# Kernel optimization log

Hardware: AMD Instinct MI355X
Metric: run time of the kernel (lower is better)

## Reference

```python
import jax, jax.numpy as jnp
import numpy as np

B = 65536      # batch of scenarios
IN = 16        # input_size
HL = 10        # hl_dim
NL = 3         # hl_num
T = 200        # number of time points
NPOP = 8.6e6   # population N


def setup_inputs() -> dict:
    key = jax.random.key(0)
    k0, k1, k2, k3 = jax.random.split(key, 4)
    data = jax.random.normal(k0, (B, IN), dtype=jnp.float32)
    times = jnp.arange(T, dtype=jnp.float32)
    # stacked params for the 3 param nets (gamma, beta, I0); xavier-ish scale, zero bias
    W0 = jax.random.normal(k1, (3, HL, IN), dtype=jnp.float32) * np.float32(1.0 / np.sqrt(IN))
    b0 = jnp.zeros((3, HL), jnp.float32)
    Wh = jax.random.normal(k2, (3, NL, HL, HL), dtype=jnp.float32) * np.float32(1.0 / np.sqrt(HL))
    bh = jnp.zeros((3, NL, HL), jnp.float32)
    Wo = jax.random.normal(k3, (3, 1, HL), dtype=jnp.float32) * np.float32(1.0 / np.sqrt(HL))
    bo = jnp.zeros((3, 1), jnp.float32)
    return {"data": data, "times": times, "W0": W0, "b0": b0,
            "Wh": Wh, "bh": bh, "Wo": Wo, "bo": bo}


def _param_nets(x, W0, b0, Wh, bh, Wo, bo):
    # runs the 3 tiny MLPs in parallel over leading net axis n in {gamma, beta, I0}
    h = jnp.tanh(jnp.einsum('bi,nhi->nbh', x, W0) + b0[:, None, :])
    for l in range(Wh.shape[1]):
        h = jnp.tanh(jnp.einsum('nbh,nkh->nbk', h, Wh[:, l]) + bh[:, l][:, None, :])
    out = jnp.einsum('nbh,noh->nbo', h, Wo) + bo[:, None, :]   # [3, B, 1]
    return jax.nn.softplus(out[..., 0])                        # [3, B]


def _forward_sir(data, times, W0, b0, Wh, bh, Wo, bo):
    vals = _param_nets(data, W0, b0, Wh, bh, Wo, bo)
    gamma, beta, I0 = vals[0], vals[1], vals[2]   # each [B]
    S0 = NPOP - I0
    R0 = jnp.zeros_like(S0)
    x0 = jnp.stack([S0, I0, R0], axis=1)          # [B, 3]

    def rhs(x):
        S, I = x[:, 0], x[:, 1]
        flux = beta * S * I / NPOP
        rec = gamma * I
        return jnp.stack([-flux, flux - rec, rec], axis=1)

    def step(x, dt):
        # classic RK4 over each interval between consecutive time points
        k1 = rhs(x)
        k2 = rhs(x + 0.5 * dt * k1)
        k3 = rhs(x + 0.5 * dt * k2)
        k4 = rhs(x + dt * k3)
        xn = x + (dt / 6.0) * (k1 + 2.0 * k2 + 2.0 * k3 + k4)
        return xn, xn

    dts = times[1:] - times[:-1]                  # [T-1]
    _, ys = jax.lax.scan(step, x0, dts)           # [T-1, B, 3]
    ys = jnp.concatenate([x0[None], ys], axis=0)  # [T, B, 3]
    return ys[:, :, 1:2].reshape(-1, 1)           # infected compartment, (T*B, output_size=1)


def reference(data, times, W0, b0, Wh, bh, Wo, bo):
    return _forward_sir(data, times, W0, b0, Wh, bh, Wo, bo)
```

## Files before the change

### kernel.cpp

```cpp
#include <hip/hip_runtime.h>
#include <math.h>

#define BSZ   65536
#define INP   16
#define HL    10
#define NL    3
#define TT    200
#define NPOP  8600000.0f

#define NCH8  24

__device__ __forceinline__ float fast_tanh(float x) {
    float e = exp2f(x * 2.8853900817779268f);
    return 1.0f - 2.0f * __builtin_amdgcn_rcpf(e + 1.0f);
}

__global__ __launch_bounds__(256) void mlp_kernel(
    const float* __restrict__ data,
    const float* __restrict__ W0,
    const float* __restrict__ b0,
    const float* __restrict__ Wh,
    const float* __restrict__ bh,
    const float* __restrict__ Wo,
    const float* __restrict__ bo,
    float* __restrict__ vals)
{
    const int n   = blockIdx.y;
    const int tid = threadIdx.x;

    __shared__ float sW0[HL * INP];
    __shared__ float sb0[HL];
    __shared__ float sWh[NL * HL * HL];
    __shared__ float sbh[NL * HL];
    __shared__ float sWo[HL];
    __shared__ float sbo;

    for (int i = tid; i < HL * INP;      i += 256) sW0[i] = W0[n * HL * INP + i];
    for (int i = tid; i < HL;            i += 256) sb0[i] = b0[n * HL + i];
    for (int i = tid; i < NL * HL * HL;  i += 256) sWh[i] = Wh[n * NL * HL * HL + i];
    for (int i = tid; i < NL * HL;       i += 256) sbh[i] = bh[n * NL * HL + i];
    for (int i = tid; i < HL;            i += 256) sWo[i] = Wo[n * HL + i];
    if (tid == 0) sbo = bo[n];
    __syncthreads();

    const int b = blockIdx.x * 256 + tid;

    float x[INP];
    const float4* xin = reinterpret_cast<const float4*>(data + (size_t)b * INP);
    #pragma unroll
    for (int q = 0; q < INP / 4; ++q) {
        float4 v = xin[q];
        x[q * 4 + 0] = v.x; x[q * 4 + 1] = v.y;
        x[q * 4 + 2] = v.z; x[q * 4 + 3] = v.w;
    }

    float h[HL];
    #pragma unroll
    for (int k = 0; k < HL; ++k) {
        float acc = sb0[k];
        #pragma unroll
        for (int i = 0; i < INP; ++i)
            acc = fmaf(x[i], sW0[k * INP + i], acc);
        h[k] = fast_tanh(acc);
    }
    #pragma unroll
    for (int l = 0; l < NL; ++l) {
        float h2[HL];
        #pragma unroll
        for (int k = 0; k < HL; ++k) {
            float acc = sbh[l * HL + k];
            #pragma unroll
            for (int i = 0; i < HL; ++i)
                acc = fmaf(h[i], sWh[(l * HL + k) * HL + i], acc);
            h2[k] = fast_tanh(acc);
        }
        #pragma unroll
        for (int k = 0; k < HL; ++k) h[k] = h2[k];
    }
    float acc = sbo;
    #pragma unroll
    for (int i = 0; i < HL; ++i)
        acc = fmaf(h[i], sWo[i], acc);

    vals[(size_t)n * BSZ + b] = fmaxf(acc, 0.0f) + log1pf(expf(-fabsf(acc)));
}

__global__ __launch_bounds__(256, 1) void sir_kernel(
    const float* __restrict__ vals,
    const float* __restrict__ times,
    float* __restrict__ out)
{
    const int tid = threadIdx.x;
    const int b = blockIdx.x * 256 + tid;

    const float gamma = vals[b];
    const float beta  = vals[BSZ + b];
    const float I0    = vals[2 * BSZ + b];

    __shared__ float sdt[208];
    if (tid < TT - 1)       sdt[tid] = times[tid + 1] - times[tid];
    else if (tid < 208)     sdt[tid] = 0.0f;
    __syncthreads();

    float S = NPOP - I0;
    float I = I0;
    const float bn = beta * (1.0f / NPOP);

    out[b] = I;

    auto step = [&](float dt) {
        const float hdt = 0.5f * dt;
        float f1 = (bn * S) * I;
        float r1 = gamma * I;
        float m1 = f1 - r1;
        float aS = fmaf(-hdt, f1, S), aI = fmaf(hdt, m1, I);
        float f2 = (bn * aS) * aI;
        float r2 = gamma * aI;
        float m2 = f2 - r2;
        float bS = fmaf(-hdt, f2, S), bI = fmaf(hdt, m2, I);
        float f3 = (bn * bS) * bI;
        float r3 = gamma * bI;
        float m3 = f3 - r3;
        float cS = fmaf(-dt, f3, S),  cI = fmaf(dt, m3, I);
        float f4 = (bn * cS) * cI;
        float r4 = gamma * cI;
        float m4 = f4 - r4;
        const float c6 = dt * (1.0f / 6.0f);
        S = fmaf(-c6, (f1 + f4) + 2.0f * (f2 + f3), S);
        I = fmaf( c6, (m1 + m4) + 2.0f * (m2 + m3), I);
    };

    const float4* sdt4 = reinterpret_cast<const float4*>(sdt);

    float4 da = sdt4[0];
    float4 db = sdt4[1];
    float* op = out + BSZ;

    #pragma unroll 1
    for (int g = 0; g < NCH8; ++g) {
        float4 na = sdt4[2 * g + 2];
        float4 nb = sdt4[2 * g + 3];
        __builtin_amdgcn_sched_barrier(0);

        float ic0, ic1, ic2, ic3, ic4, ic5, ic6, ic7;
        step(da.x); ic0 = I; op[b          ] = ic0;
        step(da.y); ic1 = I; op[b + 1 * BSZ] = ic1;
        step(da.z); ic2 = I; op[b + 2 * BSZ] = ic2;
        step(da.w); ic3 = I; op[b + 3 * BSZ] = ic3;
        step(db.x); ic4 = I; op[b + 4 * BSZ] = ic4;
        step(db.y); ic5 = I; op[b + 5 * BSZ] = ic5;
        step(db.z); ic6 = I; op[b + 6 * BSZ] = ic6;
        step(db.w); ic7 = I; op[b + 7 * BSZ] = ic7;

        asm volatile("" :: "v"(ic0), "v"(ic1), "v"(ic2), "v"(ic3),
                           "v"(ic4), "v"(ic5), "v"(ic6), "v"(ic7));

        da = na; db = nb;
        op += 8 * BSZ;
    }

    {
        float d0 = sdt[192], d1 = sdt[193], d2 = sdt[194], d3 = sdt[195];
        float d4 = sdt[196], d5 = sdt[197], d6 = sdt[198];
        float ic0, ic1, ic2, ic3, ic4, ic5, ic6;
        step(d0); ic0 = I; op[b          ] = ic0;
        step(d1); ic1 = I; op[b + 1 * BSZ] = ic1;
        step(d2); ic2 = I; op[b + 2 * BSZ] = ic2;
        step(d3); ic3 = I; op[b + 3 * BSZ] = ic3;
        step(d4); ic4 = I; op[b + 4 * BSZ] = ic4;
        step(d5); ic5 = I; op[b + 5 * BSZ] = ic5;
        step(d6); ic6 = I; op[b + 6 * BSZ] = ic6;
        asm volatile("" :: "v"(ic0), "v"(ic1), "v"(ic2), "v"(ic3),
                           "v"(ic4), "v"(ic5), "v"(ic6));
    }
}

extern "C" void kernel_launch(void* const* d_in, const int* in_sizes, int n_in,
                              void* d_out, int out_size, void* d_ws, size_t ws_size,
                              hipStream_t stream) {
    const float* data  = (const float*)d_in[0];
    const float* times = (const float*)d_in[1];
    const float* W0    = (const float*)d_in[2];
    const float* b0    = (const float*)d_in[3];
    const float* Wh    = (const float*)d_in[4];
    const float* bh    = (const float*)d_in[5];
    const float* Wo    = (const float*)d_in[6];
    const float* bo    = (const float*)d_in[7];
    float* out  = (float*)d_out;
    float* vals = (float*)d_ws;

    dim3 gridA(BSZ / 256, 3);
    mlp_kernel<<<gridA, 256, 0, stream>>>(data, W0, b0, Wh, bh, Wo, bo, vals);
    sir_kernel<<<BSZ / 256, 256, 0, stream>>>(vals, times, out);
}
```

Baseline: 32.00 us.

## Double-buffer SIR output stores with inline-asm global stores and manual vmcnt waits

Replaces the 8-step store loop with two alternating 16-step banks. Each bank has precomputed per-row offsets and issues stores as inline-asm global_store_dword with an SGPR base. Explicit s_waitcnt vmcnt(16) lets up to 16 stores stay in flight while the next bank's RK4 steps compute, and per-store address arithmetic is removed. The cost is more VGPR pressure (32 offsets plus 32 held values) and fragile hand-managed memory counters and offset wraparound.

```diff
diff --git a/kernel.cpp b/kernel.cpp
--- a/kernel.cpp
+++ b/kernel.cpp
@@ -7,8 +7,7 @@
 #define NL    3
 #define TT    200
 #define NPOP  8600000.0f
-
-#define NCH8  24
+#define ROWB  (BSZ * 4u)
 
 __device__ __forceinline__ float fast_tanh(float x) {
     float e = exp2f(x * 2.8853900817779268f);
@@ -17,12 +16,9 @@
 
 __global__ __launch_bounds__(256) void mlp_kernel(
     const float* __restrict__ data,
-    const float* __restrict__ W0,
-    const float* __restrict__ b0,
-    const float* __restrict__ Wh,
-    const float* __restrict__ bh,
-    const float* __restrict__ Wo,
-    const float* __restrict__ bo,
+    const float* __restrict__ W0,  const float* __restrict__ b0,
+    const float* __restrict__ Wh,  const float* __restrict__ bh,
+    const float* __restrict__ Wo,  const float* __restrict__ bo,
     float* __restrict__ vals)
 {
     const int n   = blockIdx.y;
@@ -84,6 +80,16 @@
 
     vals[(size_t)n * BSZ + b] = fmaxf(acc, 0.0f) + log1pf(expf(-fabsf(acc)));
 }
+
+#define ST(VOFF, VAL) \
+    asm volatile("global_store_dword %0, %1, %2" \
+                 :: "v"(VOFF), "v"(VAL), "s"(out) : "memory")
+
+#define KEEP16(A) \
+    asm volatile("" :: "v"(A[0]),  "v"(A[1]),  "v"(A[2]),  "v"(A[3]),  \
+                       "v"(A[4]),  "v"(A[5]),  "v"(A[6]),  "v"(A[7]),  \
+                       "v"(A[8]),  "v"(A[9]),  "v"(A[10]), "v"(A[11]), \
+                       "v"(A[12]), "v"(A[13]), "v"(A[14]), "v"(A[15]))
 
 __global__ __launch_bounds__(256, 1) void sir_kernel(
     const float* __restrict__ vals,
@@ -132,47 +138,89 @@
 
     const float4* sdt4 = reinterpret_cast<const float4*>(sdt);
 
-    float4 da = sdt4[0];
-    float4 db = sdt4[1];
-    float* op = out + BSZ;
+    const unsigned vb = (unsigned)b * 4u;
+    unsigned voffA[16], voffB[16];
+    #pragma unroll
+    for (int k = 0; k < 16; ++k) {
+        voffA[k] = (unsigned)(k + 1  - 32) * ROWB + vb;
+        voffB[k] = (unsigned)(k + 17 - 32) * ROWB + vb;
+    }
+    float icA[16], icB[16];
+    #pragma unroll
+    for (int k = 0; k < 16; ++k) { icA[k] = 0.0f; icB[k] = 0.0f; }
+
+    float4 d0 = sdt4[0], d1 = sdt4[1], d2 = sdt4[2], d3 = sdt4[3];
+    float4 e0, e1, e2, e3;
 
     #pragma unroll 1
-    for (int g = 0; g < NCH8; ++g) {
-        float4 na = sdt4[2 * g + 2];
-        float4 nb = sdt4[2 * g + 3];
-        __builtin_amdgcn_sched_barrier(0);
-
-        float ic0, ic1, ic2, ic3, ic4, ic5, ic6, ic7;
-        step(da.x); ic0 = I; op[b          ] = ic0;
-        step(da.y); ic1 = I; op[b + 1 * BSZ] = ic1;
-        step(da.z); ic2 = I; op[b + 2 * BSZ] = ic2;
-        step(da.w); ic3 = I; op[b + 3 * BSZ] = ic3;
-        step(db.x); ic4 = I; op[b + 4 * BSZ] = ic4;
-        step(db.y); ic5 = I; op[b + 5 * BSZ] = ic5;
-        step(db.z); ic6 = I; op[b + 6 * BSZ] = ic6;
-        step(db.w); ic7 = I; op[b + 7 * BSZ] = ic7;
-
-        asm volatile("" :: "v"(ic0), "v"(ic1), "v"(ic2), "v"(ic3),
-                           "v"(ic4), "v"(ic5), "v"(ic6), "v"(ic7));
-
-        da = na; db = nb;
-        op += 8 * BSZ;
-    }
-
-    {
-        float d0 = sdt[192], d1 = sdt[193], d2 = sdt[194], d3 = sdt[195];
-        float d4 = sdt[196], d5 = sdt[197], d6 = sdt[198];
-        float ic0, ic1, ic2, ic3, ic4, ic5, ic6;
-        step(d0); ic0 = I; op[b          ] = ic0;
-        step(d1); ic1 = I; op[b + 1 * BSZ] = ic1;
-        step(d2); ic2 = I; op[b + 2 * BSZ] = ic2;
-        step(d3); ic3 = I; op[b + 3 * BSZ] = ic3;
-        step(d4); ic4 = I; op[b + 4 * BSZ] = ic4;
-        step(d5); ic5 = I; op[b + 5 * BSZ] = ic5;
-        step(d6); ic6 = I; op[b + 6 * BSZ] = ic6;
-        asm volatile("" :: "v"(ic0), "v"(ic1), "v"(ic2), "v"(ic3),
-                           "v"(ic4), "v"(ic5), "v"(ic6));
-    }
+    for (int j = 0; j < 6; ++j) {
+        asm volatile("s_waitcnt vmcnt(16)" ::: "memory");
+        KEEP16(icA);
+        __builtin_amdgcn_sched_barrier(0);
+        #pragma unroll
+        for (int k = 0; k < 16; ++k) voffA[k] += 32u * ROWB;
+        e0 = sdt4[8 * j + 4]; e1 = sdt4[8 * j + 5];
+        e2 = sdt4[8 * j + 6]; e3 = sdt4[8 * j + 7];
+        __builtin_amdgcn_sched_barrier(0);
+
+        step(d0.x); icA[0]  = I; ST(voffA[0],  icA[0]);
+        step(d0.y); icA[1]  = I; ST(voffA[1],  icA[1]);
+        step(d0.z); icA[2]  = I; ST(voffA[2],  icA[2]);
+        step(d0.w); icA[3]  = I; ST(voffA[3],  icA[3]);
+        step(d1.x); icA[4]  = I; ST(voffA[4],  icA[4]);
+        step(d1.y); icA[5]  = I; ST(voffA[5],  icA[5]);
+        step(d1.z); icA[6]  = I; ST(voffA[6],  icA[6]);
+        step(d1.w); icA[7]  = I; ST(voffA[7],  icA[7]);
+        step(d2.x); icA[8]  = I; ST(voffA[8],  icA[8]);
+        step(d2.y); icA[9]  = I; ST(voffA[9],  icA[9]);
+        step(d2.z); icA[10] = I; ST(voffA[10], icA[10]);
+        step(d2.w); icA[11] = I; ST(voffA[11], icA[11]);
+        step(d3.x); icA[12] = I; ST(voffA[12], icA[12]);
+        step(d3.y); icA[13] = I; ST(voffA[13], icA[13]);
+        step(d3.z); icA[14] = I; ST(voffA[14], icA[14]);
+        step(d3.w); icA[15] = I; ST(voffA[15], icA[15]);
+
+        asm volatile("s_waitcnt vmcnt(16)" ::: "memory");
+        KEEP16(icB);
+        __builtin_amdgcn_sched_barrier(0);
+        #pragma unroll
+        for (int k = 0; k < 16; ++k) voffB[k] += 32u * ROWB;
+        d0 = sdt4[8 * j + 8];  d1 = sdt4[8 * j + 9];
+        d2 = sdt4[8 * j + 10]; d3 = sdt4[8 * j + 11];
+        __builtin_amdgcn_sched_barrier(0);
+
+        step(e0.x); icB[0]  = I; ST(voffB[0],  icB[0]);
+        step(e0.y); icB[1]  = I; ST(voffB[1],  icB[1]);
+        step(e0.z); icB[2]  = I; ST(voffB[2],  icB[2]);
+        step(e0.w); icB[3]  = I; ST(voffB[3],  icB[3]);
+        step(e1.x); icB[4]  = I; ST(voffB[4],  icB[4]);
+        step(e1.y); icB[5]  = I; ST(voffB[5],  icB[5]);
+        step(e1.z); icB[6]  = I; ST(voffB[6],  icB[6]);
+        step(e1.w); icB[7]  = I; ST(voffB[7],  icB[7]);
+        step(e2.x); icB[8]  = I; ST(voffB[8],  icB[8]);
+        step(e2.y); icB[9]  = I; ST(voffB[9],  icB[9]);
+        step(e2.z); icB[10] = I; ST(voffB[10], icB[10]);
+        step(e2.w); icB[11] = I; ST(voffB[11], icB[11]);
+        step(e3.x); icB[12] = I; ST(voffB[12], icB[12]);
+        step(e3.y); icB[13] = I; ST(voffB[13], icB[13]);
+        step(e3.z); icB[14] = I; ST(voffB[14], icB[14]);
+        step(e3.w); icB[15] = I; ST(voffB[15], icB[15]);
+    }
+
+    asm volatile("s_waitcnt vmcnt(0)" ::: "memory");
+    KEEP16(icA);
+    KEEP16(icB);
+    __builtin_amdgcn_sched_barrier(0);
+    #pragma unroll
+    for (int k = 0; k < 7; ++k) voffA[k] += 32u * ROWB;
+
+    step(d0.x); icA[0] = I; ST(voffA[0], icA[0]);
+    step(d0.y); icA[1] = I; ST(voffA[1], icA[1]);
+    step(d0.z); icA[2] = I; ST(voffA[2], icA[2]);
+    step(d0.w); icA[3] = I; ST(voffA[3], icA[3]);
+    step(d1.x); icA[4] = I; ST(voffA[4], icA[4]);
+    step(d1.y); icA[5] = I; ST(voffA[5], icA[5]);
+    step(d1.z); icA[6] = I; ST(voffA[6], icA[6]);
 }
 
 extern "C" void kernel_launch(void* const* d_in, const int* in_sizes, int n_in,
```

Result: no change. 31.93 us (-0.2%).

## Stage SIR outputs through double-buffered LDS and emit dwordx4 global stores

Applied to the files above, without the earlier changes.

The SIR kernel now writes each thread's per-step infected value into a double-buffered shared-memory tile of 16 time steps. After a block barrier, each wave reads its transposed slice and issues 128-bit global stores through inline assembly, replacing per-step scalar 4-byte stores. The goal is fewer store instructions and wider memory transactions on this write-heavy kernel. In exchange it adds barriers, LDS traffic and hand-placed waitcnt fences whose correctness depends on exact counter accounting.

```diff
diff --git a/kernel.cpp b/kernel.cpp
--- a/kernel.cpp
+++ b/kernel.cpp
@@ -7,8 +7,11 @@
 #define NL    3
 #define TT    200
 #define NPOP  8600000.0f
-
-#define NCH8  24
+#define ROWB  (BSZ * 4u)
+#define CH    16
+#define NCH   12
+
+typedef float f32x4 __attribute__((ext_vector_type(4)));
 
 __device__ __forceinline__ float fast_tanh(float x) {
     float e = exp2f(x * 2.8853900817779268f);
@@ -17,12 +20,9 @@
 
 __global__ __launch_bounds__(256) void mlp_kernel(
     const float* __restrict__ data,
-    const float* __restrict__ W0,
-    const float* __restrict__ b0,
-    const float* __restrict__ Wh,
-    const float* __restrict__ bh,
-    const float* __restrict__ Wo,
-    const float* __restrict__ bo,
+    const float* __restrict__ W0,  const float* __restrict__ b0,
+    const float* __restrict__ Wh,  const float* __restrict__ bh,
+    const float* __restrict__ Wo,  const float* __restrict__ bo,
     float* __restrict__ vals)
 {
     const int n   = blockIdx.y;
@@ -85,28 +85,40 @@
     vals[(size_t)n * BSZ + b] = fmaxf(acc, 0.0f) + log1pf(expf(-fabsf(acc)));
 }
 
+#define ST4(VOFF, VAL) \
+    asm volatile("global_store_dwordx4 %0, %1, %2" \
+                 :: "v"(VOFF), "v"(VAL), "s"(out) : "memory")
+
 __global__ __launch_bounds__(256, 1) void sir_kernel(
     const float* __restrict__ vals,
     const float* __restrict__ times,
     float* __restrict__ out)
 {
     const int tid = threadIdx.x;
-    const int b = blockIdx.x * 256 + tid;
+    const int b   = blockIdx.x * 256 + tid;
+    const int w   = tid >> 6;
+    const int l   = tid & 63;
 
     const float gamma = vals[b];
     const float beta  = vals[BSZ + b];
     const float I0    = vals[2 * BSZ + b];
 
     __shared__ float sdt[208];
-    if (tid < TT - 1)       sdt[tid] = times[tid + 1] - times[tid];
-    else if (tid < 208)     sdt[tid] = 0.0f;
+    __shared__ float sbuf[2][CH][256];
+
+    if (tid < TT - 1)   sdt[tid] = times[tid + 1] - times[tid];
+    else if (tid < 208) sdt[tid] = 0.0f;
     __syncthreads();
 
     float S = NPOP - I0;
     float I = I0;
     const float bn = beta * (1.0f / NPOP);
 
-    out[b] = I;
+    {
+        unsigned v0 = (unsigned)b * 4u;
+        asm volatile("global_store_dword %0, %1, %2"
+                     :: "v"(v0), "v"(I), "s"(out) : "memory");
+    }
 
     auto step = [&](float dt) {
         const float hdt = 0.5f * dt;
@@ -132,47 +144,113 @@
 
     const float4* sdt4 = reinterpret_cast<const float4*>(sdt);
 
-    float4 da = sdt4[0];
-    float4 db = sdt4[1];
-    float* op = out + BSZ;
+    const unsigned colb = ((unsigned)blockIdx.x * 256u + 4u * (unsigned)l) * 4u;
+    unsigned voff0 = (unsigned)(4 * w + 1) * ROWB + colb;
+    unsigned voff1 = voff0 + ROWB;
+    unsigned voff2 = voff0 + 2u * ROWB;
+    unsigned voff3 = voff0 + 3u * ROWB;
+
+    float4 d0 = sdt4[0], d1 = sdt4[1], d2 = sdt4[2], d3 = sdt4[3];
+    float4 e0, e1, e2, e3;
 
     #pragma unroll 1
-    for (int g = 0; g < NCH8; ++g) {
-        float4 na = sdt4[2 * g + 2];
-        float4 nb = sdt4[2 * g + 3];
-        __builtin_amdgcn_sched_barrier(0);
-
-        float ic0, ic1, ic2, ic3, ic4, ic5, ic6, ic7;
-        step(da.x); ic0 = I; op[b          ] = ic0;
-        step(da.y); ic1 = I; op[b + 1 * BSZ] = ic1;
-        step(da.z); ic2 = I; op[b + 2 * BSZ] = ic2;
-        step(da.w); ic3 = I; op[b + 3 * BSZ] = ic3;
-        step(db.x); ic4 = I; op[b + 4 * BSZ] = ic4;
-        step(db.y); ic5 = I; op[b + 5 * BSZ] = ic5;
-        step(db.z); ic6 = I; op[b + 6 * BSZ] = ic6;
-        step(db.w); ic7 = I; op[b + 7 * BSZ] = ic7;
-
-        asm volatile("" :: "v"(ic0), "v"(ic1), "v"(ic2), "v"(ic3),
-                           "v"(ic4), "v"(ic5), "v"(ic6), "v"(ic7));
-
-        da = na; db = nb;
-        op += 8 * BSZ;
-    }
-
-    {
-        float d0 = sdt[192], d1 = sdt[193], d2 = sdt[194], d3 = sdt[195];
-        float d4 = sdt[196], d5 = sdt[197], d6 = sdt[198];
-        float ic0, ic1, ic2, ic3, ic4, ic5, ic6;
-        step(d0); ic0 = I; op[b          ] = ic0;
-        step(d1); ic1 = I; op[b + 1 * BSZ] = ic1;
-        step(d2); ic2 = I; op[b + 2 * BSZ] = ic2;
-        step(d3); ic3 = I; op[b + 3 * BSZ] = ic3;
-        step(d4); ic4 = I; op[b + 4 * BSZ] = ic4;
-        step(d5); ic5 = I; op[b + 5 * BSZ] = ic5;
-        step(d6); ic6 = I; op[b + 6 * BSZ] = ic6;
-        asm volatile("" :: "v"(ic0), "v"(ic1), "v"(ic2), "v"(ic3),
-                           "v"(ic4), "v"(ic5), "v"(ic6));
-    }
+    for (int cc = 0; cc < NCH / 2; ++cc) {
+        step(d0.x); sbuf[0][ 0][tid] = I;
+        step(d0.y); sbuf[0][ 1][tid] = I;
+        step(d0.z); sbuf[0][ 2][tid] = I;
+        step(d0.w); sbuf[0][ 3][tid] = I;
+        step(d1.x); sbuf[0][ 4][tid] = I;
+        step(d1.y); sbuf[0][ 5][tid] = I;
+        step(d1.z); sbuf[0][ 6][tid] = I;
+        step(d1.w); sbuf[0][ 7][tid] = I;
+        step(d2.x); sbuf[0][ 8][tid] = I;
+        step(d2.y); sbuf[0][ 9][tid] = I;
+        step(d2.z); sbuf[0][10][tid] = I;
+        step(d2.w); sbuf[0][11][tid] = I;
+        step(d3.x); sbuf[0][12][tid] = I;
+        step(d3.y); sbuf[0][13][tid] = I;
+        step(d3.z); sbuf[0][14][tid] = I;
+        step(d3.w); sbuf[0][15][tid] = I;
+
+        asm volatile("s_waitcnt lgkmcnt(0)" ::: "memory");
+        __builtin_amdgcn_sched_barrier(0);
+        __builtin_amdgcn_s_barrier();
+
+        e0 = sdt4[8 * cc + 4]; e1 = sdt4[8 * cc + 5];
+        e2 = sdt4[8 * cc + 6]; e3 = sdt4[8 * cc + 7];
+
+        asm volatile("s_waitcnt vmcnt(4)" ::: "memory");
+        __builtin_amdgcn_sched_barrier(0);
+
+        f32x4 sA0 = *(const f32x4*)&sbuf[0][4 * w + 0][4 * l];
+        f32x4 sA1 = *(const f32x4*)&sbuf[0][4 * w + 1][4 * l];
+        f32x4 sA2 = *(const f32x4*)&sbuf[0][4 * w + 2][4 * l];
+        f32x4 sA3 = *(const f32x4*)&sbuf[0][4 * w + 3][4 * l];
+        ST4(voff0, sA0);
+        ST4(voff1, sA1);
+        ST4(voff2, sA2);
+        ST4(voff3, sA3);
+        voff0 += CH * ROWB; voff1 += CH * ROWB;
+        voff2 += CH * ROWB; voff3 += CH * ROWB;
+
+        step(e0.x); sbuf[1][ 0][tid] = I;
+        step(e0.y); sbuf[1][ 1][tid] = I;
+        step(e0.z); sbuf[1][ 2][tid] = I;
+        step(e0.w); sbuf[1][ 3][tid] = I;
+        step(e1.x); sbuf[1][ 4][tid] = I;
+        step(e1.y); sbuf[1][ 5][tid] = I;
+        step(e1.z); sbuf[1][ 6][tid] = I;
+        step(e1.w); sbuf[1][ 7][tid] = I;
+        step(e2.x); sbuf[1][ 8][tid] = I;
+        step(e2.y); sbuf[1][ 9][tid] = I;
+        step(e2.z); sbuf[1][10][tid] = I;
+        step(e2.w); sbuf[1][11][tid] = I;
+        step(e3.x); sbuf[1][12][tid] = I;
+        step(e3.y); sbuf[1][13][tid] = I;
+        step(e3.z); sbuf[1][14][tid] = I;
+        step(e3.w); sbuf[1][15][tid] = I;
+
+        asm volatile("s_waitcnt lgkmcnt(0)" ::: "memory");
+        __builtin_amdgcn_sched_barrier(0);
+        __builtin_amdgcn_s_barrier();
+
+        d0 = sdt4[8 * cc + 8];  d1 = sdt4[8 * cc + 9];
+        d2 = sdt4[8 * cc + 10]; d3 = sdt4[8 * cc + 11];
+
+        asm volatile("s_waitcnt vmcnt(4)" ::: "memory");
+        __builtin_amdgcn_sched_barrier(0);
+
+        f32x4 sB0 = *(const f32x4*)&sbuf[1][4 * w + 0][4 * l];
+        f32x4 sB1 = *(const f32x4*)&sbuf[1][4 * w + 1][4 * l];
+        f32x4 sB2 = *(const f32x4*)&sbuf[1][4 * w + 2][4 * l];
+        f32x4 sB3 = *(const f32x4*)&sbuf[1][4 * w + 3][4 * l];
+        ST4(voff0, sB0);
+        ST4(voff1, sB1);
+        ST4(voff2, sB2);
+        ST4(voff3, sB3);
+        voff0 += CH * ROWB; voff1 += CH * ROWB;
+        voff2 += CH * ROWB; voff3 += CH * ROWB;
+    }
+
+    step(d0.x); sbuf[0][0][tid] = I;
+    step(d0.y); sbuf[0][1][tid] = I;
+    step(d0.z); sbuf[0][2][tid] = I;
+    step(d0.w); sbuf[0][3][tid] = I;
+    step(d1.x); sbuf[0][4][tid] = I;
+    step(d1.y); sbuf[0][5][tid] = I;
+    step(d1.z); sbuf[0][6][tid] = I;
+
+    asm volatile("s_waitcnt lgkmcnt(0)" ::: "memory");
+    __builtin_amdgcn_sched_barrier(0);
+    __builtin_amdgcn_s_barrier();
+
+    asm volatile("s_waitcnt vmcnt(4)" ::: "memory");
+    __builtin_amdgcn_sched_barrier(0);
+
+    if (4 * w + 0 < 7) { f32x4 v = *(const f32x4*)&sbuf[0][4 * w + 0][4 * l]; ST4(voff0, v); }
+    if (4 * w + 1 < 7) { f32x4 v = *(const f32x4*)&sbuf[0][4 * w + 1][4 * l]; ST4(voff1, v); }
+    if (4 * w + 2 < 7) { f32x4 v = *(const f32x4*)&sbuf[0][4 * w + 2][4 * l]; ST4(voff2, v); }
+    if (4 * w + 3 < 7) { f32x4 v = *(const f32x4*)&sbuf[0][4 * w + 3][4 * l]; ST4(voff3, v); }
 }
 
 extern "C" void kernel_launch(void* const* d_in, const int* in_sizes, int n_in,
```

Result: slower. 32.91 us (+2.8%).

## Fold beta/N into SIR state, shrink SIR blocks to one wave, fast softplus

Applied to the files above, without the earlier changes.

The RK4 step now tracks P = beta/N * S instead of S, so each flux is a single multiply and the recovery term folds into an FMA. This cuts the per-stage instruction count. SIR blocks drop from 256 to 64 threads (one wavefront) to spread 1024 blocks across CUs, and softplus uses exp2/log2 intrinsics. The initial store uses inline asm with a 32-bit offset, and the reformulation slightly changes floating-point rounding.

```diff
diff --git a/kernel.cpp b/kernel.cpp
--- a/kernel.cpp
+++ b/kernel.cpp
@@ -15,14 +15,16 @@
     return 1.0f - 2.0f * __builtin_amdgcn_rcpf(e + 1.0f);
 }
 
+__device__ __forceinline__ float fast_softplus(float x) {
+    float t = exp2f(-fabsf(x) * 1.4426950408889634f);
+    return fmaxf(x, 0.0f) + 0.6931471805599453f * log2f(1.0f + t);
+}
+
 __global__ __launch_bounds__(256) void mlp_kernel(
     const float* __restrict__ data,
-    const float* __restrict__ W0,
-    const float* __restrict__ b0,
-    const float* __restrict__ Wh,
-    const float* __restrict__ bh,
-    const float* __restrict__ Wo,
-    const float* __restrict__ bo,
+    const float* __restrict__ W0,  const float* __restrict__ b0,
+    const float* __restrict__ Wh,  const float* __restrict__ bh,
+    const float* __restrict__ Wo,  const float* __restrict__ bo,
     float* __restrict__ vals)
 {
     const int n   = blockIdx.y;
@@ -82,80 +84,90 @@
     for (int i = 0; i < HL; ++i)
         acc = fmaf(h[i], sWo[i], acc);
 
-    vals[(size_t)n * BSZ + b] = fmaxf(acc, 0.0f) + log1pf(expf(-fabsf(acc)));
-}
-
-__global__ __launch_bounds__(256, 1) void sir_kernel(
+    vals[(size_t)n * BSZ + b] = fast_softplus(acc);
+}
+
+__global__ __launch_bounds__(64, 1) void sir_kernel(
     const float* __restrict__ vals,
     const float* __restrict__ times,
     float* __restrict__ out)
 {
     const int tid = threadIdx.x;
-    const int b = blockIdx.x * 256 + tid;
-
-    const float gamma = vals[b];
-    const float beta  = vals[BSZ + b];
-    const float I0    = vals[2 * BSZ + b];
+    const int b   = blockIdx.x * 64 + tid;
+
+    const float g    = vals[b];
+    const float beta = vals[BSZ + b];
+    const float I0   = vals[2 * BSZ + b];
 
     __shared__ float sdt[208];
-    if (tid < TT - 1)       sdt[tid] = times[tid + 1] - times[tid];
-    else if (tid < 208)     sdt[tid] = 0.0f;
+    for (int i = tid; i < 208; i += 64)
+        sdt[i] = (i < TT - 1) ? (times[i + 1] - times[i]) : 0.0f;
     __syncthreads();
 
-    float S = NPOP - I0;
+    const float bn = beta * (1.0f / NPOP);
     float I = I0;
-    const float bn = beta * (1.0f / NPOP);
-
-    out[b] = I;
+    float P = bn * (NPOP - I0);
+
+    {
+        unsigned v0 = (unsigned)b * 4u;
+        asm volatile("global_store_dword %0, %1, %2"
+                     :: "v"(v0), "v"(I), "s"(out) : "memory");
+    }
 
     auto step = [&](float dt) {
         const float hdt = 0.5f * dt;
-        float f1 = (bn * S) * I;
-        float r1 = gamma * I;
-        float m1 = f1 - r1;
-        float aS = fmaf(-hdt, f1, S), aI = fmaf(hdt, m1, I);
-        float f2 = (bn * aS) * aI;
-        float r2 = gamma * aI;
-        float m2 = f2 - r2;
-        float bS = fmaf(-hdt, f2, S), bI = fmaf(hdt, m2, I);
-        float f3 = (bn * bS) * bI;
-        float r3 = gamma * bI;
-        float m3 = f3 - r3;
-        float cS = fmaf(-dt, f3, S),  cI = fmaf(dt, m3, I);
-        float f4 = (bn * cS) * cI;
-        float r4 = gamma * cI;
-        float m4 = f4 - r4;
-        const float c6 = dt * (1.0f / 6.0f);
-        S = fmaf(-c6, (f1 + f4) + 2.0f * (f2 + f3), S);
-        I = fmaf( c6, (m1 + m4) + 2.0f * (m2 + m3), I);
+        const float hb  = bn * hdt;
+        const float db  = bn * dt;
+        const float c6  = dt * (1.0f / 6.0f);
+        const float cb  = bn * c6;
+        float f1 = P * I;
+        float m1 = fmaf(-g, I, f1);
+        float aP = fmaf(-hb, f1, P);
+        float aI = fmaf(hdt, m1, I);
+        float f2 = aP * aI;
+        float m2 = fmaf(-g, aI, f2);
+        float bP = fmaf(-hb, f2, P);
+        float bI = fmaf(hdt, m2, I);
+        float f3 = bP * bI;
+        float m3 = fmaf(-g, bI, f3);
+        float cP = fmaf(-db, f3, P);
+        float cI = fmaf(dt, m3, I);
+        float f4 = cP * cI;
+        float m4 = fmaf(-g, cI, f4);
+        float s1 = m1 + m4;
+        float s2 = m2 + m3;
+        float u1 = f1 + f4;
+        float u2 = f2 + f3;
+        I = fmaf(c6, fmaf(2.0f, s2, s1), I);
+        P = fmaf(-cb, fmaf(2.0f, u2, u1), P);
     };
 
     const float4* sdt4 = reinterpret_cast<const float4*>(sdt);
 
     float4 da = sdt4[0];
-    float4 db = sdt4[1];
+    float4 db4 = sdt4[1];
     float* op = out + BSZ;
 
     #pragma unroll 1
-    for (int g = 0; g < NCH8; ++g) {
-        float4 na = sdt4[2 * g + 2];
-        float4 nb = sdt4[2 * g + 3];
+    for (int gch = 0; gch < NCH8; ++gch) {
+        float4 na = sdt4[2 * gch + 2];
+        float4 nb = sdt4[2 * gch + 3];
         __builtin_amdgcn_sched_barrier(0);
 
         float ic0, ic1, ic2, ic3, ic4, ic5, ic6, ic7;
-        step(da.x); ic0 = I; op[b          ] = ic0;
-        step(da.y); ic1 = I; op[b + 1 * BSZ] = ic1;
-        step(da.z); ic2 = I; op[b + 2 * BSZ] = ic2;
-        step(da.w); ic3 = I; op[b + 3 * BSZ] = ic3;
-        step(db.x); ic4 = I; op[b + 4 * BSZ] = ic4;
-        step(db.y); ic5 = I; op[b + 5 * BSZ] = ic5;
-        step(db.z); ic6 = I; op[b + 6 * BSZ] = ic6;
-        step(db.w); ic7 = I; op[b + 7 * BSZ] = ic7;
+        step(da.x);  ic0 = I; op[b          ] = ic0;
+        step(da.y);  ic1 = I; op[b + 1 * BSZ] = ic1;
+        step(da.z);  ic2 = I; op[b + 2 * BSZ] = ic2;
+        step(da.w);  ic3 = I; op[b + 3 * BSZ] = ic3;
+        step(db4.x); ic4 = I; op[b + 4 * BSZ] = ic4;
+        step(db4.y); ic5 = I; op[b + 5 * BSZ] = ic5;
+        step(db4.z); ic6 = I; op[b + 6 * BSZ] = ic6;
+        step(db4.w); ic7 = I; op[b + 7 * BSZ] = ic7;
 
         asm volatile("" :: "v"(ic0), "v"(ic1), "v"(ic2), "v"(ic3),
                            "v"(ic4), "v"(ic5), "v"(ic6), "v"(ic7));
 
-        da = na; db = nb;
+        da = na; db4 = nb;
         op += 8 * BSZ;
     }
 
@@ -191,5 +203,5 @@
 
     dim3 gridA(BSZ / 256, 3);
     mlp_kernel<<<gridA, 256, 0, stream>>>(data, W0, b0, Wh, bh, Wo, bo, vals);
-    sir_kernel<<<BSZ / 256, 256, 0, stream>>>(vals, times, out);
-}
+    sir_kernel<<<BSZ / 64, 64, 0, stream>>>(vals, times, out);
+}
```

After: 30.72 us. 4.0% less time.
